# Kernel tuning notes

Hardware: AMD Instinct MI355X
Metric: run time of the kernel (lower is better)

## Reference

```python
import jax, jax.numpy as jnp
import numpy as np

N_E = 1024
E_DIM = 256
N_TOK = 65536
BETA = 0.25


def setup_inputs() -> dict:
    key = jax.random.key(0)
    k1, k2 = jax.random.split(key)
    z = jax.random.normal(k1, (N_TOK, E_DIM), dtype=jnp.float32)
    # nn.Embedding weight, init uniform(-1/n_e, 1/n_e) in the original; use normal-like scale via uniform
    W = jax.random.uniform(k2, (N_E, E_DIM), dtype=jnp.float32, minval=-1.0 / N_E, maxval=1.0 / N_E)
    return {"z": z, "W": W}


def reference(z, W):
    # cosine distance: d = -normalize(z) @ normalize(W).T  -> (N, n_e)
    zn = z / jnp.linalg.norm(z, axis=-1, keepdims=True)
    Wn = W / jnp.linalg.norm(W, axis=-1, keepdims=True)
    d = -jnp.einsum('nd,ed->ne', zn, Wn)
    min_idx = jnp.argmin(d, axis=1)                       # (N,)
    z_q = W[min_idx]                                       # (N, e_dim)
    # commitment / codebook loss with straight-through style detaches
    loss = jnp.mean((jax.lax.stop_gradient(z) - z_q) ** 2) \
         + BETA * jnp.mean((z - jax.lax.stop_gradient(z_q)) ** 2)
    # pos_indices = unique(min_idx) (sorted); neg = np.delete(arange(n_e), pos) (sorted)
    # emb = cat(W[pos], W[neg]); reproduce with a stable argsort on membership mask
    pos_mask = jnp.zeros((N_E,), dtype=bool).at[min_idx].set(True)
    order = jnp.argsort(jnp.logical_not(pos_mask), stable=True)  # pos (sorted) first, then neg (sorted)
    emb = W[order]                                         # (n_e, e_dim)
    label = pos_mask[order].astype(z.dtype)                # (n_e,)
    return emb, label, loss
```

## Files before the change

### kernel.cpp

```cpp
#include <hip/hip_runtime.h>
#include <hip/hip_bf16.h>
#include <hip/hip_fp16.h>
#include <math.h>


typedef unsigned short u16;
typedef unsigned int   u32;
typedef unsigned long long u64;
typedef __attribute__((ext_vector_type(8))) _Float16 f16x8;
typedef __attribute__((ext_vector_type(4))) float f32x4;

#define N_E   1024
#define E_DIM 256
#define N_TOK 65536
#define BETA  0.25f
#define CAPL  24
#define CAPG  8
#define D_ADM 0.025f
#define D_FIL 0.026f

#define WS_INVNORM 0
#define WS_NORMW   4096
#define WS_MASK    8192
#define WS_LACC    12288
#define WS_WCNT    14336
#define WS_WCNT2   14340
#define WS_WSW     16384
#define WS_CNT     540672
#define WS_CAND    802816
#define WS_WLIST   1851392
#define WS_WLIST2  2113536

static __device__ __forceinline__ u32 pk2fh(float a, float b) {
    __half2 p = __float22half2_rn(make_float2(a, b));
    return *reinterpret_cast<u32*>(&p);
}
static __device__ __forceinline__ u32 keyenc(float f) {
    u32 u = __float_as_uint(f);
    return u ^ (u32)(((int)u >> 31) | 0x80000000);
}
static __device__ __forceinline__ float keydec(u32 k) {
    u32 u = (k & 0x80000000u) ? (k ^ 0x80000000u) : ~k;
    return __uint_as_float(u);
}

__global__ void k_prep(const float* __restrict__ W, u16* __restrict__ Wsw,
                       float* __restrict__ inv_norm, float* __restrict__ normW,
                       int* __restrict__ mask, double* __restrict__ lacc,
                       u32* __restrict__ wcnt, u32* __restrict__ wcnt2) {
    const int n = blockIdx.x;
    const int l = threadIdx.x;
    const float4 v = reinterpret_cast<const float4*>(W + (size_t)n * E_DIM)[l];
    float s = v.x * v.x + v.y * v.y + v.z * v.z + v.w * v.w;
#pragma unroll
    for (int sh = 1; sh < 64; sh <<= 1) s += __shfl_xor(s, sh, 64);
    const float nw = sqrtf(s), inv = 1.0f / nw;
    if (l == 0) {
        inv_norm[n] = inv; normW[n] = nw; mask[n] = 0;
        if (n < 256) lacc[n] = 0.0;
        if (n == 0) { *wcnt = 0u; *wcnt2 = 0u; }
    }
    const int o = l >> 1;
    const int kc = o >> 2, q = o & 3;
    const size_t base =
        (((((size_t)(n >> 7) * 8 + kc) * 8 + ((n >> 4) & 7)) * 64 +
          (q * 16 + (n & 15))) * 8) + (l & 1) * 4;
    u32* dst = reinterpret_cast<u32*>(Wsw + base);
    dst[0] = pk2fh(v.x * inv, v.y * inv);
    dst[1] = pk2fh(v.z * inv, v.w * inv);
}

__global__ __launch_bounds__(512, 4)
void k_score(const float* __restrict__ z, const u16* __restrict__ Wsw,
             const float* __restrict__ normW, u16* __restrict__ cand_g,
             u32* __restrict__ cnt_g, int* __restrict__ mask,
             u32* __restrict__ wlist, u32* __restrict__ wcnt,
             u32* __restrict__ wlist2, u32* __restrict__ wcnt2,
             double* __restrict__ lacc) {
    __shared__ __align__(16) u16 A_sw[32768];
    __shared__ u32 bestk[128];
    __shared__ u32 cnt[128];
    __shared__ u32 slots[128 * CAPL];

    const int t    = threadIdx.x;
    const int lane = t & 63;
    const int w    = t >> 6;
    const size_t tok_base = (size_t)blockIdx.x * 128;

    if (t < 128) { bestk[t] = 0u; cnt[t] = 0u; }

    float ssq = 0.f;
#pragma unroll
    for (int i = 0; i < 8; i++) {
        const int m = ((i & 1) << 6) | (w << 3) | (lane & 7);
        const int o = ((i >> 1) << 3) | (lane >> 3);
        const float* zp = z + (tok_base + m) * E_DIM + o * 8;
        const float4 v0 = reinterpret_cast<const float4*>(zp)[0];
        const float4 v1 = reinterpret_cast<const float4*>(zp)[1];
        ssq += v0.x * v0.x + v0.y * v0.y + v0.z * v0.z + v0.w * v0.w
             + v1.x * v1.x + v1.y * v1.y + v1.z * v1.z + v1.w * v1.w;
        uint4 d;
        d.x = pk2fh(v0.x, v0.y);
        d.y = pk2fh(v0.z, v0.w);
        d.z = pk2fh(v1.x, v1.y);
        d.w = pk2fh(v1.z, v1.w);
        const int kc = o >> 2, q = o & 3, col = m & 15, mt = m >> 4;
        *reinterpret_cast<uint4*>(A_sw + ((size_t)((kc * 8 + mt) * 64 + q * 16 + col)) * 8) = d;
    }
#pragma unroll
    for (int sh = 1; sh < 64; sh <<= 1) ssq += __shfl_xor(ssq, sh, 64);
    if (lane == 0) atomicAdd(&lacc[(blockIdx.x * 8 + w) & 255], (double)ssq);
    __syncthreads();

    const int mq = w >> 2;
    const int nq = w & 3;
    const int q = lane >> 4, col = lane & 15;
    const u16* wb = Wsw + ((size_t)((nq >> 1) * 64 + (nq & 1) * 4)) * 512
                        + (size_t)lane * 8;

    f32x4 acc[4][4];

#define ZERO_ACC() { _Pragma("unroll") for (int mi = 0; mi < 4; mi++) \
    _Pragma("unroll") for (int ni = 0; ni < 4; ni++) { \
        f32x4 zf = {0.f, 0.f, 0.f, 0.f}; acc[mi][ni] = zf; } }

#define KLOOP(NB2) { \
    __builtin_amdgcn_s_setprio(1); \
    _Pragma("unroll 4") \
    for (int kc = 0; kc < 8; kc++) { \
        f16x8 bf[4], af[4]; \
        _Pragma("unroll") for (int ni = 0; ni < 4; ni++) \
            bf[ni] = *reinterpret_cast<const f16x8*>( \
                wb + (size_t)((NB2) * 128 + kc * 8 + ni) * 512); \
        _Pragma("unroll") for (int mi = 0; mi < 4; mi++) \
            af[mi] = *reinterpret_cast<const f16x8*>( \
                A_sw + ((size_t)((kc * 8 + mq * 4 + mi) * 64 + lane)) * 8); \
        _Pragma("unroll") for (int mi = 0; mi < 4; mi++) \
        _Pragma("unroll") for (int ni = 0; ni < 4; ni++) \
            acc[mi][ni] = __builtin_amdgcn_mfma_f32_16x16x32_f16( \
                af[mi], bf[ni], acc[mi][ni], 0, 0, 0); } \
    __builtin_amdgcn_s_setprio(0); }

#define ADMIT(NB2, DO_MAX) { \
    _Pragma("unroll") for (int mi = 0; mi < 4; mi++) \
    _Pragma("unroll") for (int r = 0; r < 4; r++) { \
        const int tk = mq * 64 + mi * 16 + q * 4 + r; \
        const float thr = keydec(bestk[tk]) - D_ADM; \
        const float vmax = fmaxf(fmaxf(acc[mi][0][r], acc[mi][1][r]), \
                                 fmaxf(acc[mi][2][r], acc[mi][3][r])); \
        if (vmax >= thr) { \
            if (DO_MAX) atomicMax(&bestk[tk], keyenc(vmax)); \
            _Pragma("unroll") for (int ni = 0; ni < 4; ni++) { \
                const float v = acc[mi][ni][r]; \
                if (v >= thr) { \
                    const int code = ((NB2) * 16 + nq * 4 + ni) * 16 + col; \
                    const u32 sl = atomicAdd(&cnt[tk], 1u); \
                    if (sl < CAPL) { \
                        const float vc = fminf(fmaxf((v + 16.f) * 2048.f, 0.f), 65535.f); \
                        slots[tk * CAPL + sl] = ((u32)vc << 16) | (u32)code; \
                    } } } } } }

    ZERO_ACC();
    KLOOP(0);
#pragma unroll
    for (int mi = 0; mi < 4; mi++)
#pragma unroll
        for (int r = 0; r < 4; r++) {
            float m0 = fmaxf(fmaxf(acc[mi][0][r], acc[mi][1][r]),
                             fmaxf(acc[mi][2][r], acc[mi][3][r]));
#pragma unroll
            for (int sh = 1; sh < 16; sh <<= 1)
                m0 = fmaxf(m0, __shfl_xor(m0, sh, 64));
            if (col == 0)
                atomicMax(&bestk[mq * 64 + mi * 16 + q * 4 + r], keyenc(m0));
        }
    __syncthreads();
    ADMIT(0, 0);

#pragma unroll 1
    for (int nb2 = 1; nb2 < 4; nb2++) {
        ZERO_ACC();
        KLOOP(nb2);
        ADMIT(nb2, 1);
    }
#undef ZERO_ACC
#undef KLOOP
#undef ADMIT

    __syncthreads();
    if (t < 128) {
        const size_t tokg = tok_base + t;
        const u32 c = cnt[t];
        const float best = keydec(bestk[t]);
        bool amb = false, ovf = false;
        float xacc = 0.f;
        if (c > CAPL) {
            ovf = true;
        } else {
            const float thrf = best - D_FIL;
            u16 loc[CAPG]; u32 m = 0;
            for (u32 i = 0; i < c; i++) {
                const u32 s2 = slots[t * CAPL + i];
                const float ap = (float)(s2 >> 16) * (1.0f / 2048.0f) - 16.0f;
                if (ap >= thrf) { if (m < CAPG) loc[m] = (u16)(s2 & 0xFFFFu); m++; }
            }
            if (m == 1) {
                const int bi = loc[0];
                mask[bi] = 1;
                const float nw = normW[bi];
                xacc = fmaf(-2.0f * best, nw, nw * nw);
            } else if (m <= CAPG) {
                for (u32 i = 0; i < m; i++) cand_g[tokg * CAPG + i] = loc[i];
                cnt_g[tokg] = m; amb = true;
            } else {
                ovf = true;
            }
        }
        {
            const u64 bal = __ballot(amb);
            u32 base = 0;
            if (lane == 0 && bal) base = atomicAdd(wcnt, (u32)__popcll(bal));
            base = (u32)__shfl((int)base, 0, 64);
            if (amb) wlist[base + (u32)__popcll(bal & ((1ull << lane) - 1ull))] = (u32)tokg;
        }
        {
            const u64 bal = __ballot(ovf);
            u32 base = 0;
            if (lane == 0 && bal) base = atomicAdd(wcnt2, (u32)__popcll(bal));
            base = (u32)__shfl((int)base, 0, 64);
            if (ovf) wlist2[base + (u32)__popcll(bal & ((1ull << lane) - 1ull))] = (u32)tokg;
        }
        float xs = xacc;
#pragma unroll
        for (int sh = 1; sh < 64; sh <<= 1) xs += __shfl_xor(xs, sh, 64);
        if (lane == 0) atomicAdd(&lacc[(blockIdx.x * 2 + w) & 255], (double)xs);
    }
}

__global__ __launch_bounds__(256)
void k_pick(const float* __restrict__ z, const float* __restrict__ W,
            const float* __restrict__ inv_norm, const float* __restrict__ normW,
            const u16* __restrict__ cand_g, const u32* __restrict__ cnt_g,
            const u32* __restrict__ wlist, const u32* __restrict__ wcnt,
            const u32* __restrict__ wlist2, const u32* __restrict__ wcnt2,
            int* __restrict__ mask, double* __restrict__ lacc) {
    __shared__ float zrow[E_DIM];
    __shared__ float gbv[16], gbp[16];
    __shared__ int   gbi[16];
    const int t = threadIdx.x, lane = t & 63;
    const int gl = t & 15, grp = t >> 4;

    {
        const u32 total = *wcnt;
        float xs = 0.f;
        for (u32 i = blockIdx.x * 16 + grp; i < total; i += 1024 * 16) {
            const size_t tok = wlist[i];
            float4 zv[4];
#pragma unroll
            for (int j = 0; j < 4; j++)
                zv[j] = reinterpret_cast<const float4*>(z + tok * E_DIM)[j * 16 + gl];
            const int n_it = (int)cnt_g[tok];
            float bv = -3.4e38f, bp = 0.f;
            int bi = 0x7FFFFFFF;
#pragma unroll 1
            for (int k2 = 0; k2 < n_it; k2++) {
                const int c = (int)cand_g[tok * CAPG + k2];
                float p = 0.f;
#pragma unroll
                for (int j = 0; j < 4; j++) {
                    const float4 wv = reinterpret_cast<const float4*>(W + (size_t)c * E_DIM)[j * 16 + gl];
                    p += zv[j].x * wv.x + zv[j].y * wv.y + zv[j].z * wv.z + zv[j].w * wv.w;
                }
#pragma unroll
                for (int sh = 1; sh < 16; sh <<= 1) p += __shfl_xor(p, sh, 64);
                const float s = p * inv_norm[c];
                if (s > bv || (s == bv && c < bi)) { bv = s; bi = c; bp = p; }
            }
            if (gl == 0) {
                mask[bi] = 1;
                xs += fmaf(-2.0f, bp, normW[bi] * normW[bi]);
            }
        }
        xs += __shfl_xor(xs, 16, 64);
        xs += __shfl_xor(xs, 32, 64);
        if (lane == 0) atomicAdd(&lacc[(blockIdx.x * 4 + (t >> 6)) & 255], (double)xs);
    }

    {
        const u32 total2 = *wcnt2;
        for (u32 i = blockIdx.x; i < total2; i += 1024) {
            const size_t tok = wlist2[i];
            __syncthreads();
            zrow[t] = z[tok * E_DIM + t];
            __syncthreads();
            float4 zv[4];
#pragma unroll
            for (int j = 0; j < 4; j++)
                zv[j] = reinterpret_cast<const float4*>(zrow)[j * 16 + gl];
            float bv = -3.4e38f, bp = 0.f;
            int bi = 0x7FFFFFFF;
#pragma unroll 1
            for (int k2 = 0; k2 < 64; k2 += 2) {
                const int c0 = grp * 64 + k2, c1 = c0 + 1;
                float p0 = 0.f, p1 = 0.f;
#pragma unroll
                for (int j = 0; j < 4; j++) {
                    const float4 w0 = reinterpret_cast<const float4*>(W + (size_t)c0 * E_DIM)[j * 16 + gl];
                    const float4 w1 = reinterpret_cast<const float4*>(W + (size_t)c1 * E_DIM)[j * 16 + gl];
                    p0 += zv[j].x * w0.x + zv[j].y * w0.y + zv[j].z * w0.z + zv[j].w * w0.w;
                    p1 += zv[j].x * w1.x + zv[j].y * w1.y + zv[j].z * w1.z + zv[j].w * w1.w;
                }
#pragma unroll
                for (int sh = 1; sh < 16; sh <<= 1) {
                    p0 += __shfl_xor(p0, sh, 64);
                    p1 += __shfl_xor(p1, sh, 64);
                }
                const float s0 = p0 * inv_norm[c0];
                const float s1 = p1 * inv_norm[c1];
                if (s0 > bv || (s0 == bv && c0 < bi)) { bv = s0; bi = c0; bp = p0; }
                if (s1 > bv || (s1 == bv && c1 < bi)) { bv = s1; bi = c1; bp = p1; }
            }
            if (gl == 0) { gbv[grp] = bv; gbi[grp] = bi; gbp[grp] = bp; }
            __syncthreads();
            if (t == 0) {
                float fb = gbv[0], fp = gbp[0];
                int fi = gbi[0];
                for (int g2 = 1; g2 < 16; g2++) {
                    const float v2 = gbv[g2];
                    const int i2 = gbi[g2];
                    if (v2 > fb || (v2 == fb && i2 < fi)) { fb = v2; fi = i2; fp = gbp[g2]; }
                }
                mask[fi] = 1;
                atomicAdd(&lacc[tok & 255],
                          (double)fmaf(-2.0f, fp, normW[fi] * normW[fi]));
            }
        }
    }
}

__global__ __launch_bounds__(256)
void k_emit(const float* __restrict__ W, const int* __restrict__ mask,
            const double* __restrict__ lacc, float* __restrict__ out) {
    __shared__ int    redp[256], redt[256];
    __shared__ double dred[256];
    const int e = blockIdx.x;
    const int t = threadIdx.x;
    const int4 mv = reinterpret_cast<const int4*>(mask)[t];
    const int b = t * 4;
    redt[t] = mv.x + mv.y + mv.z + mv.w;
    redp[t] = (b + 0 < e ? mv.x : 0) + (b + 1 < e ? mv.y : 0) +
              (b + 2 < e ? mv.z : 0) + (b + 3 < e ? mv.w : 0);
    if (e == 0) dred[t] = lacc[t];
    __syncthreads();
#pragma unroll
    for (int s2 = 128; s2 > 0; s2 >>= 1) {
        if (t < s2) {
            redp[t] += redp[t + s2];
            redt[t] += redt[t + s2];
            if (e == 0) dred[t] += dred[t + s2];
        }
        __syncthreads();
    }
    const int prefix = redp[0], total = redt[0];
    const int m = mask[e];
    const int r = m ? prefix : (total + e - prefix);
    out[(size_t)r * E_DIM + t] = W[(size_t)e * E_DIM + t];
    if (t == 0) out[(size_t)N_E * E_DIM + r] = m ? 1.0f : 0.0f;
    if (e == 0 && t == 0) {
        const double mse = dred[0] / (double)((size_t)N_TOK * E_DIM);
        out[(size_t)N_E * E_DIM + N_E] = (float)((1.0 + (double)BETA) * mse);
    }
}

extern "C" void kernel_launch(void* const* d_in, const int* in_sizes, int n_in,
                              void* d_out, int out_size, void* d_ws, size_t ws_size,
                              hipStream_t stream) {
    const float* z = (const float*)d_in[0];
    const float* W = (const float*)d_in[1];
    float* out = (float*)d_out;
    char* ws = (char*)d_ws;

    float*  inv_norm = (float*)(ws + WS_INVNORM);
    float*  normW    = (float*)(ws + WS_NORMW);
    int*    mask     = (int*)(ws + WS_MASK);
    double* lacc     = (double*)(ws + WS_LACC);
    u32*    wcnt     = (u32*)(ws + WS_WCNT);
    u32*    wcnt2    = (u32*)(ws + WS_WCNT2);
    u16*    Wsw      = (u16*)(ws + WS_WSW);
    u32*    cnt      = (u32*)(ws + WS_CNT);
    u16*    cand     = (u16*)(ws + WS_CAND);
    u32*    wlist    = (u32*)(ws + WS_WLIST);
    u32*    wlist2   = (u32*)(ws + WS_WLIST2);

    k_prep <<<N_E, 64, 0, stream>>>(W, Wsw, inv_norm, normW, mask, lacc,
                                    wcnt, wcnt2);
    k_score<<<N_TOK / 128, 512, 0, stream>>>(z, Wsw, normW, cand, cnt, mask,
                                             wlist, wcnt, wlist2, wcnt2, lacc);
    k_pick <<<1024, 256, 0, stream>>>(z, W, inv_norm, normW, cand, cnt,
                                      wlist, wcnt, wlist2, wcnt2, mask, lacc);
    k_emit <<<N_E, 256, 0, stream>>>(W, mask, lacc, out);
}
```

Baseline: 150.5 us.

## Switch scoring GEMM to 32x32x16 MFMA tiles with matching operand layouts

Replaces the 16x16x32 f16 MFMA tiling in the scoring kernel with 32x32x16 MFMA, changing the swizzled layouts of both the normalized codebook and the staged token tile and remapping accumulator rows to tokens. Larger MFMA tiles halve the operand fragment loads per FLOP and use fewer instructions, reducing LDS/global load pressure in the K loop. The row-max reduction now spans 32 lanes and per-row admission work touches more accumulator registers. k_prep is also repacked to process four codebook rows per 256-thread block, which cuts the launch to fewer, larger blocks.

```diff
diff --git a/kernel.cpp b/kernel.cpp
--- a/kernel.cpp
+++ b/kernel.cpp
@@ -8,7 +8,7 @@
 typedef unsigned int   u32;
 typedef unsigned long long u64;
 typedef __attribute__((ext_vector_type(8))) _Float16 f16x8;
-typedef __attribute__((ext_vector_type(4))) float f32x4;
+typedef __attribute__((ext_vector_type(16))) float f32x16;
 
 #define N_E   1024
 #define E_DIM 256
@@ -44,12 +44,14 @@
     return __uint_as_float(u);
 }
 
-__global__ void k_prep(const float* __restrict__ W, u16* __restrict__ Wsw,
-                       float* __restrict__ inv_norm, float* __restrict__ normW,
-                       int* __restrict__ mask, double* __restrict__ lacc,
-                       u32* __restrict__ wcnt, u32* __restrict__ wcnt2) {
-    const int n = blockIdx.x;
-    const int l = threadIdx.x;
+__global__ __launch_bounds__(256)
+void k_prep(const float* __restrict__ W, u16* __restrict__ Wsw,
+            float* __restrict__ inv_norm, float* __restrict__ normW,
+            int* __restrict__ mask, double* __restrict__ lacc,
+            u32* __restrict__ wcnt, u32* __restrict__ wcnt2) {
+    const int t = threadIdx.x;
+    const int n = blockIdx.x * 4 + (t >> 6);
+    const int l = t & 63;
     const float4 v = reinterpret_cast<const float4*>(W + (size_t)n * E_DIM)[l];
     float s = v.x * v.x + v.y * v.y + v.z * v.z + v.w * v.w;
 #pragma unroll
@@ -60,11 +62,11 @@
         if (n < 256) lacc[n] = 0.0;
         if (n == 0) { *wcnt = 0u; *wcnt2 = 0u; }
     }
-    const int o = l >> 1;
-    const int kc = o >> 2, q = o & 3;
+    const int o  = l >> 1;
+    const int ks = o >> 1, hi = o & 1;
     const size_t base =
-        (((((size_t)(n >> 7) * 8 + kc) * 8 + ((n >> 4) & 7)) * 64 +
-          (q * 16 + (n & 15))) * 8) + (l & 1) * 4;
+        (((size_t)(n >> 8) * 128 + ((n >> 6) & 3) * 32 + ((n >> 5) & 1) * 16 + ks) * 64
+         + hi * 32 + (n & 31)) * 8 + (l & 1) * 4;
     u32* dst = reinterpret_cast<u32*>(Wsw + base);
     dst[0] = pk2fh(v.x * inv, v.y * inv);
     dst[1] = pk2fh(v.z * inv, v.w * inv);
@@ -104,8 +106,11 @@
         d.y = pk2fh(v0.z, v0.w);
         d.z = pk2fh(v1.x, v1.y);
         d.w = pk2fh(v1.z, v1.w);
-        const int kc = o >> 2, q = o & 3, col = m & 15, mt = m >> 4;
-        *reinterpret_cast<uint4*>(A_sw + ((size_t)((kc * 8 + mt) * 64 + q * 16 + col)) * 8) = d;
+        const int ks = o >> 2, hi = (o >> 1) & 1;
+        const int ks2 = o >> 1, hi2 = o & 1;
+        (void)ks; (void)hi;
+        *reinterpret_cast<uint4*>(A_sw +
+            ((size_t)((ks2 * 4 + (m >> 5)) * 64 + hi2 * 32 + (m & 31))) * 8) = d;
     }
 #pragma unroll
     for (int sh = 1; sh < 64; sh <<= 1) ssq += __shfl_xor(ssq, sh, 64);
@@ -114,46 +119,47 @@
 
     const int mq = w >> 2;
     const int nq = w & 3;
-    const int q = lane >> 4, col = lane & 15;
-    const u16* wb = Wsw + ((size_t)((nq >> 1) * 64 + (nq & 1) * 4)) * 512
-                        + (size_t)lane * 8;
-
-    f32x4 acc[4][4];
-
-#define ZERO_ACC() { _Pragma("unroll") for (int mi = 0; mi < 4; mi++) \
-    _Pragma("unroll") for (int ni = 0; ni < 4; ni++) { \
-        f32x4 zf = {0.f, 0.f, 0.f, 0.f}; acc[mi][ni] = zf; } }
+    const int hi = lane >> 5, col32 = lane & 31;
+
+    f32x16 acc[2][2];
+
+#define ZERO_ACC() { _Pragma("unroll") for (int mt = 0; mt < 2; mt++) \
+    _Pragma("unroll") for (int nt = 0; nt < 2; nt++) { \
+        f32x16 zf = {0.f,0.f,0.f,0.f,0.f,0.f,0.f,0.f, \
+                     0.f,0.f,0.f,0.f,0.f,0.f,0.f,0.f}; acc[mt][nt] = zf; } }
 
 #define KLOOP(NB2) { \
     __builtin_amdgcn_s_setprio(1); \
     _Pragma("unroll 4") \
-    for (int kc = 0; kc < 8; kc++) { \
-        f16x8 bf[4], af[4]; \
-        _Pragma("unroll") for (int ni = 0; ni < 4; ni++) \
-            bf[ni] = *reinterpret_cast<const f16x8*>( \
-                wb + (size_t)((NB2) * 128 + kc * 8 + ni) * 512); \
-        _Pragma("unroll") for (int mi = 0; mi < 4; mi++) \
-            af[mi] = *reinterpret_cast<const f16x8*>( \
-                A_sw + ((size_t)((kc * 8 + mq * 4 + mi) * 64 + lane)) * 8); \
-        _Pragma("unroll") for (int mi = 0; mi < 4; mi++) \
-        _Pragma("unroll") for (int ni = 0; ni < 4; ni++) \
-            acc[mi][ni] = __builtin_amdgcn_mfma_f32_16x16x32_f16( \
-                af[mi], bf[ni], acc[mi][ni], 0, 0, 0); } \
+    for (int ks = 0; ks < 16; ks++) { \
+        f16x8 bf[2], af[2]; \
+        _Pragma("unroll") for (int nt = 0; nt < 2; nt++) \
+            bf[nt] = *reinterpret_cast<const f16x8*>( \
+                Wsw + (size_t)((NB2) * 128 + nq * 32 + nt * 16 + ks) * 512 \
+                    + (size_t)lane * 8); \
+        _Pragma("unroll") for (int mt = 0; mt < 2; mt++) \
+            af[mt] = *reinterpret_cast<const f16x8*>( \
+                A_sw + ((size_t)((ks * 4 + mq * 2 + mt) * 64 + lane)) * 8); \
+        _Pragma("unroll") for (int mt = 0; mt < 2; mt++) \
+        _Pragma("unroll") for (int nt = 0; nt < 2; nt++) \
+            acc[mt][nt] = __builtin_amdgcn_mfma_f32_32x32x16_f16( \
+                af[mt], bf[nt], acc[mt][nt], 0, 0, 0); } \
     __builtin_amdgcn_s_setprio(0); }
 
+#define TKOF(MT, RG) (mq * 64 + (MT) * 32 + ((RG) & 3) + (((RG) >> 2) << 3) + (hi << 2))
+
 #define ADMIT(NB2, DO_MAX) { \
-    _Pragma("unroll") for (int mi = 0; mi < 4; mi++) \
-    _Pragma("unroll") for (int r = 0; r < 4; r++) { \
-        const int tk = mq * 64 + mi * 16 + q * 4 + r; \
+    _Pragma("unroll") for (int mt = 0; mt < 2; mt++) \
+    _Pragma("unroll") for (int rg = 0; rg < 16; rg++) { \
+        const int tk = TKOF(mt, rg); \
         const float thr = keydec(bestk[tk]) - D_ADM; \
-        const float vmax = fmaxf(fmaxf(acc[mi][0][r], acc[mi][1][r]), \
-                                 fmaxf(acc[mi][2][r], acc[mi][3][r])); \
+        const float vmax = fmaxf(acc[mt][0][rg], acc[mt][1][rg]); \
         if (vmax >= thr) { \
             if (DO_MAX) atomicMax(&bestk[tk], keyenc(vmax)); \
-            _Pragma("unroll") for (int ni = 0; ni < 4; ni++) { \
-                const float v = acc[mi][ni][r]; \
+            _Pragma("unroll") for (int nt = 0; nt < 2; nt++) { \
+                const float v = acc[mt][nt][rg]; \
                 if (v >= thr) { \
-                    const int code = ((NB2) * 16 + nq * 4 + ni) * 16 + col; \
+                    const int code = (NB2) * 256 + nq * 64 + nt * 32 + col32; \
                     const u32 sl = atomicAdd(&cnt[tk], 1u); \
                     if (sl < CAPL) { \
                         const float vc = fminf(fmaxf((v + 16.f) * 2048.f, 0.f), 65535.f); \
@@ -163,16 +169,15 @@
     ZERO_ACC();
     KLOOP(0);
 #pragma unroll
-    for (int mi = 0; mi < 4; mi++)
-#pragma unroll
-        for (int r = 0; r < 4; r++) {
-            float m0 = fmaxf(fmaxf(acc[mi][0][r], acc[mi][1][r]),
-                             fmaxf(acc[mi][2][r], acc[mi][3][r]));
-#pragma unroll
-            for (int sh = 1; sh < 16; sh <<= 1)
+    for (int mt = 0; mt < 2; mt++)
+#pragma unroll
+        for (int rg = 0; rg < 16; rg++) {
+            float m0 = fmaxf(acc[mt][0][rg], acc[mt][1][rg]);
+#pragma unroll
+            for (int sh = 1; sh < 32; sh <<= 1)
                 m0 = fmaxf(m0, __shfl_xor(m0, sh, 64));
-            if (col == 0)
-                atomicMax(&bestk[mq * 64 + mi * 16 + q * 4 + r], keyenc(m0));
+            if (col32 == 0)
+                atomicMax(&bestk[TKOF(mt, rg)], keyenc(m0));
         }
     __syncthreads();
     ADMIT(0, 0);
@@ -186,6 +191,7 @@
 #undef ZERO_ACC
 #undef KLOOP
 #undef ADMIT
+#undef TKOF
 
     __syncthreads();
     if (t < 128) {
@@ -392,8 +398,8 @@
     u32*    wlist    = (u32*)(ws + WS_WLIST);
     u32*    wlist2   = (u32*)(ws + WS_WLIST2);
 
-    k_prep <<<N_E, 64, 0, stream>>>(W, Wsw, inv_norm, normW, mask, lacc,
-                                    wcnt, wcnt2);
+    k_prep <<<N_E / 4, 256, 0, stream>>>(W, Wsw, inv_norm, normW, mask, lacc,
+                                         wcnt, wcnt2);
     k_score<<<N_TOK / 128, 512, 0, stream>>>(z, Wsw, normW, cand, cnt, mask,
                                              wlist, wcnt, wlist2, wcnt2, lacc);
     k_pick <<<1024, 256, 0, stream>>>(z, W, inv_norm, normW, cand, cnt,
```

After: 160.5 us. 1.07x slower.

## Fuse fp32 candidate re-check into scoring kernel, dropping separate pick pass

Applied to the files above, without the earlier changes.

Moves the exact fp32 rescoring of ambiguous and overflowed tokens from a separate k_pick kernel into the tail of k_score. It uses the block's shared-memory slot lists instead of global worklists and atomics. This removes one kernel launch, the global candidate and worklist traffic, and the counter resets. The cost is that each score block now serializes its own tail work, so a block with many ambiguous or overflow tokens stalls the others. The overflow path does a full 1024-code scan with 32 groups of 16 lanes.

```diff
diff --git a/kernel.cpp b/kernel.cpp
--- a/kernel.cpp
+++ b/kernel.cpp
@@ -23,13 +23,7 @@
 #define WS_NORMW   4096
 #define WS_MASK    8192
 #define WS_LACC    12288
-#define WS_WCNT    14336
-#define WS_WCNT2   14340
 #define WS_WSW     16384
-#define WS_CNT     540672
-#define WS_CAND    802816
-#define WS_WLIST   1851392
-#define WS_WLIST2  2113536
 
 static __device__ __forceinline__ u32 pk2fh(float a, float b) {
     __half2 p = __float22half2_rn(make_float2(a, b));
@@ -46,8 +40,7 @@
 
 __global__ void k_prep(const float* __restrict__ W, u16* __restrict__ Wsw,
                        float* __restrict__ inv_norm, float* __restrict__ normW,
-                       int* __restrict__ mask, double* __restrict__ lacc,
-                       u32* __restrict__ wcnt, u32* __restrict__ wcnt2) {
+                       int* __restrict__ mask, double* __restrict__ lacc) {
     const int n = blockIdx.x;
     const int l = threadIdx.x;
     const float4 v = reinterpret_cast<const float4*>(W + (size_t)n * E_DIM)[l];
@@ -58,7 +51,6 @@
     if (l == 0) {
         inv_norm[n] = inv; normW[n] = nw; mask[n] = 0;
         if (n < 256) lacc[n] = 0.0;
-        if (n == 0) { *wcnt = 0u; *wcnt2 = 0u; }
     }
     const int o = l >> 1;
     const int kc = o >> 2, q = o & 3;
@@ -71,16 +63,18 @@
 }
 
 __global__ __launch_bounds__(512, 4)
-void k_score(const float* __restrict__ z, const u16* __restrict__ Wsw,
-             const float* __restrict__ normW, u16* __restrict__ cand_g,
-             u32* __restrict__ cnt_g, int* __restrict__ mask,
-             u32* __restrict__ wlist, u32* __restrict__ wcnt,
-             u32* __restrict__ wlist2, u32* __restrict__ wcnt2,
-             double* __restrict__ lacc) {
+void k_score(const float* __restrict__ z, const float* __restrict__ W,
+             const u16* __restrict__ Wsw,
+             const float* __restrict__ inv_norm, const float* __restrict__ normW,
+             int* __restrict__ mask, double* __restrict__ lacc) {
     __shared__ __align__(16) u16 A_sw[32768];
     __shared__ u32 bestk[128];
     __shared__ u32 cnt[128];
     __shared__ u32 slots[128 * CAPL];
+    __shared__ u32 ovfCnt;
+    __shared__ u32 ovfList[128];
+    __shared__ float gbv[32], gbp[32];
+    __shared__ int   gbi[32];
 
     const int t    = threadIdx.x;
     const int lane = t & 63;
@@ -88,6 +82,7 @@
     const size_t tok_base = (size_t)blockIdx.x * 128;
 
     if (t < 128) { bestk[t] = 0u; cnt[t] = 0u; }
+    if (t == 0) ovfCnt = 0u;
 
     float ssq = 0.f;
 #pragma unroll
@@ -189,82 +184,97 @@
 
     __syncthreads();
     if (t < 128) {
-        const size_t tokg = tok_base + t;
         const u32 c = cnt[t];
         const float best = keydec(bestk[t]);
-        bool amb = false, ovf = false;
+        u32 status = 0u;
         float xacc = 0.f;
         if (c > CAPL) {
-            ovf = true;
+            const u32 p = atomicAdd(&ovfCnt, 1u);
+            ovfList[p] = (u32)t;
+            status = 0xFFFFFFFFu;
         } else {
             const float thrf = best - D_FIL;
-            u16 loc[CAPG]; u32 m = 0;
+            u32 loc[CAPG]; u32 m = 0;
             for (u32 i = 0; i < c; i++) {
                 const u32 s2 = slots[t * CAPL + i];
                 const float ap = (float)(s2 >> 16) * (1.0f / 2048.0f) - 16.0f;
-                if (ap >= thrf) { if (m < CAPG) loc[m] = (u16)(s2 & 0xFFFFu); m++; }
+                if (ap >= thrf) { if (m < CAPG) loc[m] = s2 & 0xFFFFu; m++; }
             }
             if (m == 1) {
-                const int bi = loc[0];
+                const int bi = (int)loc[0];
                 mask[bi] = 1;
                 const float nw = normW[bi];
                 xacc = fmaf(-2.0f * best, nw, nw * nw);
             } else if (m <= CAPG) {
-                for (u32 i = 0; i < m; i++) cand_g[tokg * CAPG + i] = loc[i];
-                cnt_g[tokg] = m; amb = true;
+                for (u32 i = 0; i < m; i++) slots[t * CAPL + i] = loc[i];
+                status = m;
             } else {
-                ovf = true;
-            }
-        }
-        {
-            const u64 bal = __ballot(amb);
-            u32 base = 0;
-            if (lane == 0 && bal) base = atomicAdd(wcnt, (u32)__popcll(bal));
-            base = (u32)__shfl((int)base, 0, 64);
-            if (amb) wlist[base + (u32)__popcll(bal & ((1ull << lane) - 1ull))] = (u32)tokg;
-        }
-        {
-            const u64 bal = __ballot(ovf);
-            u32 base = 0;
-            if (lane == 0 && bal) base = atomicAdd(wcnt2, (u32)__popcll(bal));
-            base = (u32)__shfl((int)base, 0, 64);
-            if (ovf) wlist2[base + (u32)__popcll(bal & ((1ull << lane) - 1ull))] = (u32)tokg;
-        }
+                const u32 p = atomicAdd(&ovfCnt, 1u);
+                ovfList[p] = (u32)t;
+                status = 0xFFFFFFFFu;
+            }
+        }
+        cnt[t] = status;
         float xs = xacc;
 #pragma unroll
         for (int sh = 1; sh < 64; sh <<= 1) xs += __shfl_xor(xs, sh, 64);
         if (lane == 0) atomicAdd(&lacc[(blockIdx.x * 2 + w) & 255], (double)xs);
     }
-}
-
-__global__ __launch_bounds__(256)
-void k_pick(const float* __restrict__ z, const float* __restrict__ W,
-            const float* __restrict__ inv_norm, const float* __restrict__ normW,
-            const u16* __restrict__ cand_g, const u32* __restrict__ cnt_g,
-            const u32* __restrict__ wlist, const u32* __restrict__ wcnt,
-            const u32* __restrict__ wlist2, const u32* __restrict__ wcnt2,
-            int* __restrict__ mask, double* __restrict__ lacc) {
-    __shared__ float zrow[E_DIM];
-    __shared__ float gbv[16], gbp[16];
-    __shared__ int   gbi[16];
-    const int t = threadIdx.x, lane = t & 63;
-    const int gl = t & 15, grp = t >> 4;
+    __syncthreads();
 
     {
-        const u32 total = *wcnt;
-        float xs = 0.f;
-        for (u32 i = blockIdx.x * 16 + grp; i < total; i += 1024 * 16) {
-            const size_t tok = wlist[i];
+        const int gl = t & 15, grp = t >> 4;
+#pragma unroll 1
+        for (int it = 0; it < 4; ++it) {
+            const int tk = grp * 4 + it;
+            const u32 m = cnt[tk];
+            if (m >= 2u && m <= (u32)CAPG) {
+                const size_t tok = tok_base + tk;
+                float4 zv[4];
+#pragma unroll
+                for (int j = 0; j < 4; j++)
+                    zv[j] = reinterpret_cast<const float4*>(z + tok * E_DIM)[j * 16 + gl];
+                float bv = -3.4e38f, bp = 0.f;
+                int bi = 0x7FFFFFFF;
+#pragma unroll 1
+                for (u32 k2 = 0; k2 < m; k2++) {
+                    const int c = (int)slots[tk * CAPL + k2];
+                    float p = 0.f;
+#pragma unroll
+                    for (int j = 0; j < 4; j++) {
+                        const float4 wv = reinterpret_cast<const float4*>(W + (size_t)c * E_DIM)[j * 16 + gl];
+                        p += zv[j].x * wv.x + zv[j].y * wv.y + zv[j].z * wv.z + zv[j].w * wv.w;
+                    }
+#pragma unroll
+                    for (int sh = 1; sh < 16; sh <<= 1) p += __shfl_xor(p, sh, 64);
+                    const float s = p * inv_norm[c];
+                    if (s > bv || (s == bv && c < bi)) { bv = s; bi = c; bp = p; }
+                }
+                if (gl == 0) {
+                    mask[bi] = 1;
+                    atomicAdd(&lacc[(u32)tok & 255],
+                              (double)fmaf(-2.0f, bp, normW[bi] * normW[bi]));
+                }
+            }
+        }
+    }
+
+    {
+        const int gl = t & 15, grp = t >> 4;
+        const u32 novf = ovfCnt;
+#pragma unroll 1
+        for (u32 i = 0; i < novf; ++i) {
+            const int tk = (int)ovfList[i];
+            const size_t tok = tok_base + tk;
             float4 zv[4];
 #pragma unroll
             for (int j = 0; j < 4; j++)
                 zv[j] = reinterpret_cast<const float4*>(z + tok * E_DIM)[j * 16 + gl];
-            const int n_it = (int)cnt_g[tok];
             float bv = -3.4e38f, bp = 0.f;
             int bi = 0x7FFFFFFF;
 #pragma unroll 1
-            for (int k2 = 0; k2 < n_it; k2++) {
-                const int c = (int)cand_g[tok * CAPG + k2];
+            for (int k2 = 0; k2 < 32; ++k2) {
+                const int c = grp * 32 + k2;
                 float p = 0.f;
 #pragma unroll
                 for (int j = 0; j < 4; j++) {
@@ -275,65 +285,22 @@
                 for (int sh = 1; sh < 16; sh <<= 1) p += __shfl_xor(p, sh, 64);
                 const float s = p * inv_norm[c];
                 if (s > bv || (s == bv && c < bi)) { bv = s; bi = c; bp = p; }
-            }
-            if (gl == 0) {
-                mask[bi] = 1;
-                xs += fmaf(-2.0f, bp, normW[bi] * normW[bi]);
-            }
-        }
-        xs += __shfl_xor(xs, 16, 64);
-        xs += __shfl_xor(xs, 32, 64);
-        if (lane == 0) atomicAdd(&lacc[(blockIdx.x * 4 + (t >> 6)) & 255], (double)xs);
-    }
-
-    {
-        const u32 total2 = *wcnt2;
-        for (u32 i = blockIdx.x; i < total2; i += 1024) {
-            const size_t tok = wlist2[i];
-            __syncthreads();
-            zrow[t] = z[tok * E_DIM + t];
-            __syncthreads();
-            float4 zv[4];
-#pragma unroll
-            for (int j = 0; j < 4; j++)
-                zv[j] = reinterpret_cast<const float4*>(zrow)[j * 16 + gl];
-            float bv = -3.4e38f, bp = 0.f;
-            int bi = 0x7FFFFFFF;
-#pragma unroll 1
-            for (int k2 = 0; k2 < 64; k2 += 2) {
-                const int c0 = grp * 64 + k2, c1 = c0 + 1;
-                float p0 = 0.f, p1 = 0.f;
-#pragma unroll
-                for (int j = 0; j < 4; j++) {
-                    const float4 w0 = reinterpret_cast<const float4*>(W + (size_t)c0 * E_DIM)[j * 16 + gl];
-                    const float4 w1 = reinterpret_cast<const float4*>(W + (size_t)c1 * E_DIM)[j * 16 + gl];
-                    p0 += zv[j].x * w0.x + zv[j].y * w0.y + zv[j].z * w0.z + zv[j].w * w0.w;
-                    p1 += zv[j].x * w1.x + zv[j].y * w1.y + zv[j].z * w1.z + zv[j].w * w1.w;
-                }
-#pragma unroll
-                for (int sh = 1; sh < 16; sh <<= 1) {
-                    p0 += __shfl_xor(p0, sh, 64);
-                    p1 += __shfl_xor(p1, sh, 64);
-                }
-                const float s0 = p0 * inv_norm[c0];
-                const float s1 = p1 * inv_norm[c1];
-                if (s0 > bv || (s0 == bv && c0 < bi)) { bv = s0; bi = c0; bp = p0; }
-                if (s1 > bv || (s1 == bv && c1 < bi)) { bv = s1; bi = c1; bp = p1; }
             }
             if (gl == 0) { gbv[grp] = bv; gbi[grp] = bi; gbp[grp] = bp; }
             __syncthreads();
             if (t == 0) {
                 float fb = gbv[0], fp = gbp[0];
                 int fi = gbi[0];
-                for (int g2 = 1; g2 < 16; g2++) {
+                for (int g2 = 1; g2 < 32; g2++) {
                     const float v2 = gbv[g2];
                     const int i2 = gbi[g2];
                     if (v2 > fb || (v2 == fb && i2 < fi)) { fb = v2; fi = i2; fp = gbp[g2]; }
                 }
                 mask[fi] = 1;
-                atomicAdd(&lacc[tok & 255],
+                atomicAdd(&lacc[(u32)tok & 255],
                           (double)fmaf(-2.0f, fp, normW[fi] * normW[fi]));
             }
+            __syncthreads();
         }
     }
 }
@@ -384,19 +351,10 @@
     float*  normW    = (float*)(ws + WS_NORMW);
     int*    mask     = (int*)(ws + WS_MASK);
     double* lacc     = (double*)(ws + WS_LACC);
-    u32*    wcnt     = (u32*)(ws + WS_WCNT);
-    u32*    wcnt2    = (u32*)(ws + WS_WCNT2);
     u16*    Wsw      = (u16*)(ws + WS_WSW);
-    u32*    cnt      = (u32*)(ws + WS_CNT);
-    u16*    cand     = (u16*)(ws + WS_CAND);
-    u32*    wlist    = (u32*)(ws + WS_WLIST);
-    u32*    wlist2   = (u32*)(ws + WS_WLIST2);
-
-    k_prep <<<N_E, 64, 0, stream>>>(W, Wsw, inv_norm, normW, mask, lacc,
-                                    wcnt, wcnt2);
-    k_score<<<N_TOK / 128, 512, 0, stream>>>(z, Wsw, normW, cand, cnt, mask,
-                                             wlist, wcnt, wlist2, wcnt2, lacc);
-    k_pick <<<1024, 256, 0, stream>>>(z, W, inv_norm, normW, cand, cnt,
-                                      wlist, wcnt, wlist2, wcnt2, mask, lacc);
+
+    k_prep <<<N_E, 64, 0, stream>>>(W, Wsw, inv_norm, normW, mask, lacc);
+    k_score<<<N_TOK / 128, 512, 0, stream>>>(z, W, Wsw, inv_norm, normW,
+                                             mask, lacc);
     k_emit <<<N_E, 256, 0, stream>>>(W, mask, lacc, out);
 }
```

Measured after the change: 139.3 us. -7.4%, faster.
